# Performance work log

Measured on AMD Instinct MI355X. Metric: run time of the kernel, lower is better.

## Reference

```python
import jax, jax.numpy as jnp
import numpy as np

B, S, D, F, E, R, K = 1, 512, 1024, 4096, 8, 16, 2
SCALING = 32.0 / 16.0  # lora_alpha / lora_r
EPS = 1e-6


def setup_inputs() -> dict:
    key = jax.random.key(0)
    ks = jax.random.split(key, 12)
    w = lambda k, shape: jax.random.normal(k, shape, dtype=jnp.float32) * 0.02
    return {
        "x": jax.random.normal(ks[0], (B, S, D), dtype=jnp.float32),
        "norm_w": jnp.ones((D,), jnp.float32),
        "w1": w(ks[1], (F, D)),      # up proj (gate branch)
        "w3": w(ks[2], (F, D)),      # up proj (value branch)
        "w2": w(ks[3], (D, F)),      # down proj
        "gate_w": w(ks[4], (E, D)),  # router
        "a1": w(ks[5], (E, R, D)), "b1": w(ks[6], (E, F, R)),
        "a3": w(ks[7], (E, R, D)), "b3": w(ks[8], (E, F, R)),
        "a2": w(ks[9], (E, R, F)), "b2": w(ks[10], (E, D, R)),
    }


def _forward(x, norm_w, w1, w3, w2, gate_w, a1, b1, a3, b3, a2, b2):
    Bq, Sq, Dq = x.shape
    # RMSNorm
    nx = x * jax.lax.rsqrt(jnp.mean(x * x, axis=-1, keepdims=True) + EPS) * norm_w
    t = nx.reshape(-1, Dq)  # [T, D] flattened tokens
    # Mixtral-style routing: softmax -> top-k -> renormalize
    probs = jax.nn.softmax(t @ gate_w.T, axis=-1)          # [T, E]
    topw, topi = jax.lax.top_k(probs, K)                   # [T, K]
    topw = topw / jnp.sum(topw, axis=-1, keepdims=True)
    weights = jnp.sum(jax.nn.one_hot(topi, E, dtype=t.dtype) * topw[..., None], axis=1)  # [T, E]
    # Shared base up-projections
    base1 = t @ w1.T  # [T, F]
    base3 = t @ w3.T  # [T, F]
    # Per-expert LoRA deltas (rank-R): [E, T, F]
    h1 = base1[None] + SCALING * jnp.einsum('etr,efr->etf', jnp.einsum('td,erd->etr', t, a1), b1)
    h3 = base3[None] + SCALING * jnp.einsum('etr,efr->etf', jnp.einsum('td,erd->etr', t, a3), b3)
    act = jax.nn.silu(h1) * h3  # SwiGLU, [E, T, F]
    # Down projection: base + per-expert LoRA -> [E, T, D]
    out_e = jnp.einsum('etf,df->etd', act, w2) \
        + SCALING * jnp.einsum('etr,edr->etd', jnp.einsum('etf,erf->etr', act, a2), b2)
    # Weighted mix over experts (weight is 0 for non-selected experts)
    out = jnp.einsum('te,etd->td', weights, out_e)
    return out.reshape(Bq, Sq, Dq)


def reference(x, norm_w, w1, w3, w2, gate_w, a1, b1, a3, b3, a2, b2):
    return _forward(x, norm_w, w1, w3, w2, gate_w, a1, b1, a3, b3, a2, b2)
```

## Files before the change

### kernel.cpp

```cpp
#include <hip/hip_runtime.h>
#include <hip/hip_bf16.h>
#include <math.h>

#define TT 512
#define DD 1024
#define FF 4096
#define EE 8
#define RR 16
#define KKSEL 2
#define SCALING 2.0f
#define EPSV 1e-6f
#define DFC 128
#define SCHUNK 32
#define CVTB 1536

typedef unsigned short u16;
typedef short bhalf8 __attribute__((ext_vector_type(8)));
typedef float floatx4 __attribute__((ext_vector_type(4)));
typedef float f32x4 __attribute__((ext_vector_type(4)));
typedef unsigned short u16x8 __attribute__((ext_vector_type(8)));

__device__ __forceinline__ u16 f2b(float f) {
    unsigned x = __builtin_bit_cast(unsigned, f);
    unsigned r = (x + 0x7fffu + ((x >> 16) & 1u)) >> 16;
    return (u16)r;
}
__device__ __forceinline__ float b2f(u16 b) {
    unsigned x = ((unsigned)b) << 16;
    return __builtin_bit_cast(float, x);
}

__device__ __forceinline__ void gl_lds16(const void* g, void* l) {
    __builtin_amdgcn_global_load_lds(
        (const __attribute__((address_space(1))) void*)g,
        (__attribute__((address_space(3))) void*)l, 16, 0, 0);
}

__global__ __launch_bounds__(256) void prep_f2b_k(const float* __restrict__ x,
                                                  const float* __restrict__ nw,
                                                  const float* __restrict__ gw,
                                                  const float* __restrict__ a1,
                                                  const float* __restrict__ a3,
                                                  const float* __restrict__ w1,
                                                  const float* __restrict__ w3,
                                                  const float* __restrict__ w2,
                                                  u16* __restrict__ tb,
                                                  float* __restrict__ topw,
                                                  int* __restrict__ topi,
                                                  float* __restrict__ s1,
                                                  float* __restrict__ s3,
                                                  u16* __restrict__ wB) {
    __shared__ float tL[DD];
    __shared__ float red[12];
    __shared__ int sE[2];
    int tid = threadIdx.x;

    if (blockIdx.x < CVTB) {
        const int FD = FF * DD;
        int bid = blockIdx.x;
        int seg = bid >> 9;
        const float* src = (seg == 0) ? w1 : ((seg == 1) ? w3 : w2);
        u16* dst = wB + (size_t)seg * FD;
        int base = (bid & 511) * 8192;
        f32x4 v[8];
        #pragma unroll
        for (int j = 0; j < 8; j++)
            v[j] = __builtin_nontemporal_load((const f32x4*)(src + base + j * 1024) + tid);
        #pragma unroll
        for (int j = 0; j < 8; j++) {
            ushort4 o = { f2b(v[j][0]), f2b(v[j][1]), f2b(v[j][2]), f2b(v[j][3]) };
            *(ushort4*)(dst + base + j * 1024 + tid * 4) = o;
        }
        return;
    }

    int tok = blockIdx.x - CVTB;
    int wave = tid >> 6, lane = tid & 63;
    const float* xr = x + (size_t)tok * DD;
    float xv[4];
    float ss = 0.f;
    #pragma unroll
    for (int i = 0; i < 4; i++) { xv[i] = xr[tid + 256 * i]; ss += xv[i] * xv[i]; }
    #pragma unroll
    for (int o = 32; o > 0; o >>= 1) ss += __shfl_down(ss, o);
    if (lane == 0) red[wave] = ss;
    __syncthreads();
    if (tid == 0) red[8] = rsqrtf((red[0] + red[1] + red[2] + red[3]) * (1.0f / DD) + EPSV);
    __syncthreads();
    float rs = red[8];
    #pragma unroll
    for (int i = 0; i < 4; i++) {
        float v = xv[i] * rs * nw[tid + 256 * i];
        tL[tid + 256 * i] = v;
        tb[(size_t)tok * DD + tid + 256 * i] = f2b(v);
    }
    __syncthreads();
    {
        const float* g0 = gw + (size_t)(2 * wave) * DD;
        const float* g1 = g0 + DD;
        float a0 = 0.f, a1v = 0.f;
        for (int d = lane; d < DD; d += 64) {
            float tv = tL[d];
            a0 = fmaf(tv, g0[d], a0);
            a1v = fmaf(tv, g1[d], a1v);
        }
        #pragma unroll
        for (int o = 32; o > 0; o >>= 1) { a0 += __shfl_down(a0, o); a1v += __shfl_down(a1v, o); }
        if (lane == 0) { red[2 * wave] = a0; red[2 * wave + 1] = a1v; }
    }
    __syncthreads();
    if (tid == 0) {
        float m = red[0];
        #pragma unroll
        for (int e = 1; e < EE; e++) m = fmaxf(m, red[e]);
        float p[EE];
        #pragma unroll
        for (int e = 0; e < EE; e++) p[e] = expf(red[e] - m);
        int i0 = 0; float v0 = p[0];
        for (int e = 1; e < EE; e++) if (p[e] > v0) { v0 = p[e]; i0 = e; }
        int i1 = -1; float v1 = -1.f;
        for (int e = 0; e < EE; e++) { if (e == i0) continue; if (p[e] > v1) { v1 = p[e]; i1 = e; } }
        float inv = 1.f / (v0 + v1);
        topi[tok * KKSEL + 0] = i0;
        topi[tok * KKSEL + 1] = i1;
        topw[tok * KKSEL + 0] = v0 * inv;
        topw[tok * KKSEL + 1] = v1 * inv;
        sE[0] = i0; sE[1] = i1;
    }
    __syncthreads();
    {
        int half = wave >> 1, ten = wave & 1;
        int slot = tok * 2 + half;
        int e = sE[half];
        const float* ap = ten ? a3 : a1;
        float* sp = ten ? s3 : s1;
        float tv[16];
        #pragma unroll
        for (int i = 0; i < 16; i++) tv[i] = tL[lane + 64 * i];
        const float* ab = ap + (size_t)e * RR * DD;
        #pragma unroll
        for (int r = 0; r < RR; r++) {
            const float* ar = ab + (size_t)r * DD;
            float c = 0.f;
            #pragma unroll
            for (int i = 0; i < 16; i++) c = fmaf(tv[i], ar[lane + 64 * i], c);
            #pragma unroll
            for (int o = 32; o > 0; o >>= 1) c += __shfl_down(c, o);
            if (lane == 0) sp[slot * RR + r] = SCALING * c;
        }
    }
}

__global__ __launch_bounds__(256) void delta_act_k(const float* __restrict__ b1,
                                                   const float* __restrict__ b3,
                                                   const float* __restrict__ s1,
                                                   const float* __restrict__ s3,
                                                   const int* __restrict__ lists,
                                                   const int* __restrict__ counts,
                                                   const u16* __restrict__ hb,
                                                   u16* __restrict__ actb) {
    int e = blockIdx.y, f0 = blockIdx.x * DFC;
    int st = blockIdx.z * SCHUNK;
    int n = counts[e];
    if (st >= n) return;
    int gn = min(SCHUNK, n - st);
    __shared__ float bL[2][16 * 132];
    __shared__ float sG[2][SCHUNK * 16];
    __shared__ int   sSlot[SCHUNK];
    int tid = threadIdx.x;
    int g = tid >> 7, f = tid & 127;
    const int* lp = lists + e * 1024 + st;
    {
        const float* bsrc1 = b1 + ((size_t)e * FF + f0) * RR;
        const float* bsrc3 = b3 + ((size_t)e * FF + f0) * RR;
        #pragma unroll
        for (int i = tid; i < DFC * 16; i += 256) {
            int fi = i >> 4, r = i & 15;
            bL[0][r * 132 + fi] = bsrc1[i];
            bL[1][r * 132 + fi] = bsrc3[i];
        }
        int sl_l = (tid & 127) >> 2, q = tid & 3;
        if (sl_l < gn) {
            int slot = lp[sl_l];
            const float* ssrc = g ? s3 : s1;
            *(float4*)&sG[g][sl_l * 16 + q * 4] = *(const float4*)&ssrc[slot * RR + q * 4];
            if (g == 0 && q == 0) sSlot[sl_l] = slot;
        }
    }
    __syncthreads();
    for (int ii = g; ii < gn; ii += 2) {
        int slot = sSlot[ii];
        int tok = slot >> 1;
        float h1b = b2f(hb[(size_t)tok * (2 * FF) + f0 + f]);
        float h3b = b2f(hb[(size_t)tok * (2 * FF) + FF + f0 + f]);
        const float* sp1 = &sG[0][ii * 16];
        const float* sp3 = &sG[1][ii * 16];
        float d1 = 0.f, d3 = 0.f;
        #pragma unroll
        for (int r = 0; r < RR; r++) {
            d1 = fmaf(sp1[r], bL[0][r * 132 + f], d1);
            d3 = fmaf(sp3[r], bL[1][r * 132 + f], d3);
        }
        float h1 = h1b + d1, h3 = h3b + d3;
        float sig = 1.f / (1.f + expf(-h1));
        actb[(size_t)slot * FF + f0 + f] = f2b(h1 * sig * h3);
    }
}

template<int SPLITK, bool BF16OUT, bool LISTS>
__global__ __launch_bounds__(256) void gemm_nt(const u16* __restrict__ A,
                                               const u16* __restrict__ B,
                                               void* __restrict__ Cv,
                                               int M, int N, int K,
                                               const int* __restrict__ topi,
                                               int* __restrict__ lists,
                                               int* __restrict__ counts) {
    __shared__ u16 As[3][64 * 32];
    __shared__ u16 Bs[3][128 * 32];
    int tid = threadIdx.x;

    if (LISTS && blockIdx.y == gridDim.y - 1) {
        if (blockIdx.x == 0) {
            int* cnt = (int*)&As[0][0];
            if (tid < EE) cnt[tid] = 0;
            __syncthreads();
            for (int s = tid; s < TT * KKSEL; s += 256) atomicAdd(&cnt[topi[s]], 1);
            __syncthreads();
            if (tid < EE) { counts[tid] = cnt[tid]; cnt[tid] = 0; }
            __syncthreads();
            for (int s = tid; s < TT * KKSEL; s += 256) {
                int e = topi[s];
                int p = atomicAdd(&cnt[e], 1);
                lists[e * 1024 + p] = s;
            }
        }
        return;
    }

    int w = tid >> 6, lane = tid & 63;
    int wr = w >> 1, wc = w & 1;
    int lr = lane & 15, ks = lane >> 4;
    int z = (SPLITK > 1) ? blockIdx.z : 0;
    int kc = K / SPLITK;
    int k0s = z * kc;
    int nk = kc / 32;
    int m0 = blockIdx.y * 64, n0 = blockIdx.x * 128;

    int row = tid >> 2;
    int inb = (tid & 3) * 16;
    size_t rb = (size_t)K * 2;
    const char* Ag  = (const char*)A + (size_t)(m0 + row) * rb + inb + (size_t)k0s * 2;
    const char* Bg  = (const char*)B + (size_t)(n0 + row) * rb + inb + (size_t)k0s * 2;
    const char* Bg2 = Bg + 64 * rb;

    floatx4 zero4 = {0.f, 0.f, 0.f, 0.f};
    floatx4 acc[2][4];
    #pragma unroll
    for (int i = 0; i < 2; i++)
        #pragma unroll
        for (int j = 0; j < 4; j++) acc[i][j] = zero4;

    auto stage = [&](int buf, int kt) {
        size_t kb = (size_t)kt * 64;
        gl_lds16(Ag + kb, &As[buf][w * 512]);
        gl_lds16(Bg + kb, &Bs[buf][w * 512]);
        gl_lds16(Bg2 + kb, &Bs[buf][2048 + w * 512]);
    };
    auto compute = [&](int buf) {
        bhalf8 af[2], bf[4];
        #pragma unroll
        for (int i = 0; i < 2; i++)
            af[i] = *(const bhalf8*)&As[buf][(wr * 32 + i * 16 + lr) * 32 + ks * 8];
        #pragma unroll
        for (int j = 0; j < 4; j++)
            bf[j] = *(const bhalf8*)&Bs[buf][(wc * 64 + j * 16 + lr) * 32 + ks * 8];
        #pragma unroll
        for (int i = 0; i < 2; i++)
            #pragma unroll
            for (int j = 0; j < 4; j++)
                acc[i][j] = __builtin_amdgcn_mfma_f32_16x16x32_bf16(af[i], bf[j], acc[i][j], 0, 0, 0);
    };

    stage(0, 0);
    stage(1, 1);
    asm volatile("s_waitcnt vmcnt(3)" ::: "memory");
    __builtin_amdgcn_s_barrier();

    int cur = 0;
    for (int kt = 0; kt < nk; ++kt) {
        int pre = cur + 2; if (pre >= 3) pre -= 3;
        if (kt + 2 < nk) stage(pre, kt + 2);
        compute(cur);
        asm volatile("s_waitcnt lgkmcnt(0)" ::: "memory");
        if (kt + 1 < nk) {
            if (kt + 2 < nk) asm volatile("s_waitcnt vmcnt(3)" ::: "memory");
            else             asm volatile("s_waitcnt vmcnt(0)" ::: "memory");
            __builtin_amdgcn_s_barrier();
        }
        cur = (cur + 1 == 3) ? 0 : cur + 1;
    }

    int crow = (lane >> 4) * 4;
    #pragma unroll
    for (int i = 0; i < 2; i++) {
        #pragma unroll
        for (int j = 0; j < 4; j++) {
            int r0 = m0 + wr * 32 + i * 16 + crow;
            int c0 = n0 + wc * 64 + j * 16 + lr;
            if (BF16OUT) {
                u16* Cb = (u16*)Cv;
                #pragma unroll
                for (int mm = 0; mm < 4; mm++)
                    Cb[(size_t)(r0 + mm) * N + c0] = f2b(acc[i][j][mm]);
            } else {
                float* Cf = (float*)Cv + (size_t)z * M * N;
                #pragma unroll
                for (int mm = 0; mm < 4; mm++)
                    Cf[(size_t)(r0 + mm) * N + c0] = acc[i][j][mm];
            }
        }
    }
}

__global__ __launch_bounds__(256) void s2mix_k(const u16* __restrict__ actb,
                                               const float* __restrict__ a2,
                                               const int* __restrict__ topi,
                                               const float* __restrict__ topw,
                                               float* __restrict__ s2,
                                               u16* __restrict__ mixedb) {
    int tok = blockIdx.x;
    int tid = threadIdx.x, wave = tid >> 6, lane = tid & 63;
    int slot = tok * 2 + (wave >> 1);
    int e = topi[slot];
    const u16* ar = actb + (size_t)slot * FF;
    float av[64];
    #pragma unroll
    for (int i = 0; i < 16; i++) {
        ushort4 u = *(const ushort4*)(ar + lane * 4 + 256 * i);
        av[i * 4 + 0] = b2f(u.x); av[i * 4 + 1] = b2f(u.y);
        av[i * 4 + 2] = b2f(u.z); av[i * 4 + 3] = b2f(u.w);
    }
    #pragma unroll
    for (int rr = 0; rr < 8; rr++) {
        int r = (wave & 1) * 8 + rr;
        const float* a2p = a2 + ((size_t)e * RR + r) * FF;
        float c = 0.f;
        #pragma unroll
        for (int i = 0; i < 16; i++) {
            float4 w4 = *(const float4*)(a2p + lane * 4 + 256 * i);
            c = fmaf(av[i * 4 + 0], w4.x, c);
            c = fmaf(av[i * 4 + 1], w4.y, c);
            c = fmaf(av[i * 4 + 2], w4.z, c);
            c = fmaf(av[i * 4 + 3], w4.w, c);
        }
        #pragma unroll
        for (int o = 32; o > 0; o >>= 1) c += __shfl_down(c, o);
        if (lane == 0) s2[slot * RR + r] = SCALING * c;
    }
    float w0 = topw[tok * 2], w1v = topw[tok * 2 + 1];
    const u16* a0 = actb + (size_t)(tok * 2) * FF;
    const u16* a1p = a0 + FF;
    #pragma unroll
    for (int it = 0; it < 2; it++) {
        int f = tid * 8 + it * 2048;
        u16x8 v0 = *(const u16x8*)(a0 + f);
        u16x8 v1 = *(const u16x8*)(a1p + f);
        u16x8 o;
        #pragma unroll
        for (int q = 0; q < 8; q++)
            o[q] = f2b(w0 * b2f(v0[q]) + w1v * b2f(v1[q]));
        *(u16x8*)(mixedb + (size_t)tok * FF + f) = o;
    }
}

__global__ __launch_bounds__(256) void combine_k(const float* __restrict__ downP,
                                                 const float* __restrict__ s2,
                                                 const float* __restrict__ b2,
                                                 const float* __restrict__ topw,
                                                 const int* __restrict__ topi,
                                                 float* __restrict__ out) {
    int tok = blockIdx.x;
    for (int d = threadIdx.x; d < DD; d += 256) {
        float v = 0.f;
        #pragma unroll
        for (int zz = 0; zz < 8; zz++)
            v += downP[(size_t)zz * TT * DD + (size_t)tok * DD + d];
        #pragma unroll
        for (int k = 0; k < KKSEL; k++) {
            int slot = tok * KKSEL + k;
            int e = topi[slot];
            float w = topw[slot];
            const float* b2p = b2 + ((size_t)e * DD + d) * RR;
            const float* s2p = s2 + slot * RR;
            float l = 0.f;
            #pragma unroll
            for (int r = 0; r < RR; r++) l = fmaf(s2p[r], b2p[r], l);
            v += w * l;
        }
        out[(size_t)tok * DD + d] = v;
    }
}

extern "C" void kernel_launch(void* const* d_in, const int* in_sizes, int n_in,
                              void* d_out, int out_size, void* d_ws, size_t ws_size,
                              hipStream_t stream) {
    const float* x  = (const float*)d_in[0];
    const float* nw = (const float*)d_in[1];
    const float* w1 = (const float*)d_in[2];
    const float* w3 = (const float*)d_in[3];
    const float* w2 = (const float*)d_in[4];
    const float* gw = (const float*)d_in[5];
    const float* a1 = (const float*)d_in[6];
    const float* b1 = (const float*)d_in[7];
    const float* a3 = (const float*)d_in[8];
    const float* b3 = (const float*)d_in[9];
    const float* a2 = (const float*)d_in[10];
    const float* b2 = (const float*)d_in[11];
    float* out = (float*)d_out;

    float* downP = (float*)d_ws;
    float* s1    = downP + (size_t)8 * TT * DD;
    float* s3    = s1 + (size_t)TT * KKSEL * RR;
    float* s2    = s3 + (size_t)TT * KKSEL * RR;
    float* topw  = s2 + (size_t)TT * KKSEL * RR;
    int*   topi  = (int*)(topw + TT * KKSEL);
    int*   lists = topi + TT * KKSEL;
    int*   counts= lists + EE * 1024;
    u16*   tb    = (u16*)(counts + 16);
    u16*   wB    = tb + (size_t)TT * DD;
    u16*   w2b   = wB + (size_t)2 * FF * DD;
    u16*   hb    = w2b + (size_t)DD * FF;
    u16*   actb  = hb + (size_t)TT * 2 * FF;
    u16*   mixedb= actb + (size_t)TT * KKSEL * FF;

    prep_f2b_k<<<CVTB + TT, 256, 0, stream>>>(
        x, nw, gw, a1, a3, w1, w3, w2, tb, topw, topi, s1, s3, wB);
    gemm_nt<1, true, true><<<dim3(2 * FF / 128, TT / 64 + 1), 256, 0, stream>>>(
        tb, wB, hb, TT, 2 * FF, DD, topi, lists, counts);
    delta_act_k<<<dim3(FF / DFC, EE, 32), 256, 0, stream>>>(
        b1, b3, s1, s3, lists, counts, hb, actb);
    s2mix_k<<<TT, 256, 0, stream>>>(actb, a2, topi, topw, s2, mixedb);
    gemm_nt<8, false, false><<<dim3(DD / 128, TT / 64, 8), 256, 0, stream>>>(
        mixedb, w2b, downP, TT, DD, FF, nullptr, nullptr, nullptr);
    combine_k<<<TT, 256, 0, stream>>>(downP, s2, b2, topw, topi, out);
}
```

Baseline: 105.5 us.

## Fuse prep, weight conversion and up-projection GEMM into one persistent dataflow kernel

Merges the RMSNorm/routing prep kernel, the fp32-to-bf16 weight conversion and the first up-projection GEMM into a single kernel. Weight conversion becomes a work queue drained by all blocks. GEMM tiles spin on per-panel completion counters and a prep-done counter, so each tile can start as soon as its weight panel is converted instead of waiting at a kernel boundary. The expert list building moves into a dedicated block. This aims to overlap conversion with compute and cut launch gaps, but it adds inter-block spin-waits that assume co-residency (deadlock risk if the blocks are not scheduled together), plus atomic traffic and a memset.

```diff
diff --git a/kernel.cpp b/kernel.cpp
--- a/kernel.cpp
+++ b/kernel.cpp
@@ -12,7 +12,7 @@
 #define EPSV 1e-6f
 #define DFC 128
 #define SCHUNK 32
-#define CVTB 1536
+#define NQITEMS 1536
 
 typedef unsigned short u16;
 typedef short bhalf8 __attribute__((ext_vector_type(8)));
@@ -36,117 +36,262 @@
         (__attribute__((address_space(3))) void*)l, 16, 0, 0);
 }
 
-__global__ __launch_bounds__(256) void prep_f2b_k(const float* __restrict__ x,
-                                                  const float* __restrict__ nw,
-                                                  const float* __restrict__ gw,
-                                                  const float* __restrict__ a1,
-                                                  const float* __restrict__ a3,
-                                                  const float* __restrict__ w1,
-                                                  const float* __restrict__ w3,
-                                                  const float* __restrict__ w2,
-                                                  u16* __restrict__ tb,
-                                                  float* __restrict__ topw,
-                                                  int* __restrict__ topi,
-                                                  float* __restrict__ s1,
-                                                  float* __restrict__ s3,
-                                                  u16* __restrict__ wB) {
-    __shared__ float tL[DD];
+__global__ __launch_bounds__(256) void fused1_k(const float* __restrict__ x,
+                                                const float* __restrict__ nw,
+                                                const float* __restrict__ gw,
+                                                const float* __restrict__ a1,
+                                                const float* __restrict__ a3,
+                                                const float* __restrict__ w1,
+                                                const float* __restrict__ w3,
+                                                const float* __restrict__ w2,
+                                                u16* __restrict__ tb,
+                                                float* __restrict__ topw,
+                                                int* __restrict__ topi,
+                                                float* __restrict__ s1,
+                                                float* __restrict__ s3,
+                                                u16* __restrict__ wB,
+                                                u16* __restrict__ hb,
+                                                int* __restrict__ flags,
+                                                int* __restrict__ lists,
+                                                int* __restrict__ counts) {
+    __shared__ u16 sh[3 * 2048 + 3 * 4096];
+    __shared__ int qItS;
     __shared__ float red[12];
     __shared__ int sE[2];
     int tid = threadIdx.x;
-
-    if (blockIdx.x < CVTB) {
+    int bid = blockIdx.x;
+    int* qHead = flags;
+    int* prepDone = flags + 1;
+    int* panelCnt = flags + 64;
+
+    auto drain_queue = [&]() {
         const int FD = FF * DD;
-        int bid = blockIdx.x;
-        int seg = bid >> 9;
-        const float* src = (seg == 0) ? w1 : ((seg == 1) ? w3 : w2);
-        u16* dst = wB + (size_t)seg * FD;
-        int base = (bid & 511) * 8192;
-        f32x4 v[8];
-        #pragma unroll
-        for (int j = 0; j < 8; j++)
-            v[j] = __builtin_nontemporal_load((const f32x4*)(src + base + j * 1024) + tid);
-        #pragma unroll
-        for (int j = 0; j < 8; j++) {
-            ushort4 o = { f2b(v[j][0]), f2b(v[j][1]), f2b(v[j][2]), f2b(v[j][3]) };
-            *(ushort4*)(dst + base + j * 1024 + tid * 4) = o;
-        }
+        for (;;) {
+            if (tid == 0) qItS = atomicAdd(qHead, 1);
+            __syncthreads();
+            int it = qItS;
+            __syncthreads();
+            if (it >= NQITEMS) break;
+            const float* src;
+            u16* dst;
+            int p = -1;
+            if (it < 1024) {
+                p = it >> 4;
+                int row0 = p * 128 + (it & 15) * 8;
+                src = (row0 < FF) ? (w1 + (size_t)row0 * DD) : (w3 + (size_t)(row0 - FF) * DD);
+                dst = wB + (size_t)row0 * DD;
+            } else {
+                int c = it - 1024;
+                src = w2 + (size_t)c * 8192;
+                dst = wB + (size_t)2 * FD + (size_t)c * 8192;
+            }
+            f32x4 v[8];
+            #pragma unroll
+            for (int j = 0; j < 8; j++)
+                v[j] = __builtin_nontemporal_load((const f32x4*)(src + j * 1024) + tid);
+            #pragma unroll
+            for (int j = 0; j < 8; j++) {
+                ushort4 o = { f2b(v[j][0]), f2b(v[j][1]), f2b(v[j][2]), f2b(v[j][3]) };
+                *(ushort4*)(dst + j * 1024 + tid * 4) = o;
+            }
+            __syncthreads();
+            if (p >= 0 && tid == 0)
+                __hip_atomic_fetch_add(&panelCnt[p], 1, __ATOMIC_RELEASE, __HIP_MEMORY_SCOPE_AGENT);
+        }
+    };
+
+    if (bid < TT) {
+        int tok = bid;
+        int wave = tid >> 6, lane = tid & 63;
+        float* tL = (float*)sh;
+        const float* xr = x + (size_t)tok * DD;
+        float xv[4];
+        float ss = 0.f;
+        #pragma unroll
+        for (int i = 0; i < 4; i++) { xv[i] = xr[tid + 256 * i]; ss += xv[i] * xv[i]; }
+        #pragma unroll
+        for (int o = 32; o > 0; o >>= 1) ss += __shfl_down(ss, o);
+        if (lane == 0) red[wave] = ss;
+        __syncthreads();
+        if (tid == 0) red[8] = rsqrtf((red[0] + red[1] + red[2] + red[3]) * (1.0f / DD) + EPSV);
+        __syncthreads();
+        float rs = red[8];
+        #pragma unroll
+        for (int i = 0; i < 4; i++) {
+            float v = xv[i] * rs * nw[tid + 256 * i];
+            tL[tid + 256 * i] = v;
+            tb[(size_t)tok * DD + tid + 256 * i] = f2b(v);
+        }
+        __syncthreads();
+        {
+            const float* g0 = gw + (size_t)(2 * wave) * DD;
+            const float* g1 = g0 + DD;
+            float a0 = 0.f, a1v = 0.f;
+            for (int d = lane; d < DD; d += 64) {
+                float tv = tL[d];
+                a0 = fmaf(tv, g0[d], a0);
+                a1v = fmaf(tv, g1[d], a1v);
+            }
+            #pragma unroll
+            for (int o = 32; o > 0; o >>= 1) { a0 += __shfl_down(a0, o); a1v += __shfl_down(a1v, o); }
+            if (lane == 0) { red[2 * wave] = a0; red[2 * wave + 1] = a1v; }
+        }
+        __syncthreads();
+        if (tid == 0) {
+            float m = red[0];
+            #pragma unroll
+            for (int e = 1; e < EE; e++) m = fmaxf(m, red[e]);
+            float p[EE];
+            #pragma unroll
+            for (int e = 0; e < EE; e++) p[e] = expf(red[e] - m);
+            int i0 = 0; float v0 = p[0];
+            for (int e = 1; e < EE; e++) if (p[e] > v0) { v0 = p[e]; i0 = e; }
+            int i1 = -1; float v1 = -1.f;
+            for (int e = 0; e < EE; e++) { if (e == i0) continue; if (p[e] > v1) { v1 = p[e]; i1 = e; } }
+            float inv = 1.f / (v0 + v1);
+            topi[tok * KKSEL + 0] = i0;
+            topi[tok * KKSEL + 1] = i1;
+            topw[tok * KKSEL + 0] = v0 * inv;
+            topw[tok * KKSEL + 1] = v1 * inv;
+            sE[0] = i0; sE[1] = i1;
+        }
+        __syncthreads();
+        {
+            int half = wave >> 1, ten = wave & 1;
+            int slot = tok * 2 + half;
+            int e = sE[half];
+            const float* ap = ten ? a3 : a1;
+            float* sp = ten ? s3 : s1;
+            float tv[16];
+            #pragma unroll
+            for (int i = 0; i < 16; i++) tv[i] = tL[lane + 64 * i];
+            const float* ab = ap + (size_t)e * RR * DD;
+            #pragma unroll
+            for (int r = 0; r < RR; r++) {
+                const float* ar = ab + (size_t)r * DD;
+                float c = 0.f;
+                #pragma unroll
+                for (int i = 0; i < 16; i++) c = fmaf(tv[i], ar[lane + 64 * i], c);
+                #pragma unroll
+                for (int o = 32; o > 0; o >>= 1) c += __shfl_down(c, o);
+                if (lane == 0) sp[slot * RR + r] = SCALING * c;
+            }
+        }
+        __syncthreads();
+        if (tid == 0)
+            __hip_atomic_fetch_add(prepDone, 1, __ATOMIC_RELEASE, __HIP_MEMORY_SCOPE_AGENT);
+        drain_queue();
         return;
     }
 
-    int tok = blockIdx.x - CVTB;
-    int wave = tid >> 6, lane = tid & 63;
-    const float* xr = x + (size_t)tok * DD;
-    float xv[4];
-    float ss = 0.f;
-    #pragma unroll
-    for (int i = 0; i < 4; i++) { xv[i] = xr[tid + 256 * i]; ss += xv[i] * xv[i]; }
-    #pragma unroll
-    for (int o = 32; o > 0; o >>= 1) ss += __shfl_down(ss, o);
-    if (lane == 0) red[wave] = ss;
+    if (bid == TT + 512) {
+        drain_queue();
+        if (tid == 0) {
+            while (__hip_atomic_load(prepDone, __ATOMIC_ACQUIRE, __HIP_MEMORY_SCOPE_AGENT) < TT)
+                __builtin_amdgcn_s_sleep(8);
+        }
+        __syncthreads();
+        int* cnt = (int*)sh;
+        if (tid < EE) cnt[tid] = 0;
+        __syncthreads();
+        for (int s = tid; s < TT * KKSEL; s += 256) atomicAdd(&cnt[topi[s]], 1);
+        __syncthreads();
+        if (tid < EE) { counts[tid] = cnt[tid]; cnt[tid] = 0; }
+        __syncthreads();
+        for (int s = tid; s < TT * KKSEL; s += 256) {
+            int e = topi[s];
+            int p = atomicAdd(&cnt[e], 1);
+            lists[e * 1024 + p] = s;
+        }
+        return;
+    }
+
+    drain_queue();
+    int t = bid - TT;
+    int gx = t >> 3, gy = t & 7;
+    if (tid == 0) {
+        for (;;) {
+            int pc = __hip_atomic_load(&panelCnt[gx], __ATOMIC_ACQUIRE, __HIP_MEMORY_SCOPE_AGENT);
+            int pd = __hip_atomic_load(prepDone, __ATOMIC_ACQUIRE, __HIP_MEMORY_SCOPE_AGENT);
+            if (pc >= 16 && pd >= TT) break;
+            __builtin_amdgcn_s_sleep(8);
+        }
+    }
     __syncthreads();
-    if (tid == 0) red[8] = rsqrtf((red[0] + red[1] + red[2] + red[3]) * (1.0f / DD) + EPSV);
-    __syncthreads();
-    float rs = red[8];
-    #pragma unroll
-    for (int i = 0; i < 4; i++) {
-        float v = xv[i] * rs * nw[tid + 256 * i];
-        tL[tid + 256 * i] = v;
-        tb[(size_t)tok * DD + tid + 256 * i] = f2b(v);
-    }
-    __syncthreads();
-    {
-        const float* g0 = gw + (size_t)(2 * wave) * DD;
-        const float* g1 = g0 + DD;
-        float a0 = 0.f, a1v = 0.f;
-        for (int d = lane; d < DD; d += 64) {
-            float tv = tL[d];
-            a0 = fmaf(tv, g0[d], a0);
-            a1v = fmaf(tv, g1[d], a1v);
-        }
-        #pragma unroll
-        for (int o = 32; o > 0; o >>= 1) { a0 += __shfl_down(a0, o); a1v += __shfl_down(a1v, o); }
-        if (lane == 0) { red[2 * wave] = a0; red[2 * wave + 1] = a1v; }
-    }
-    __syncthreads();
-    if (tid == 0) {
-        float m = red[0];
-        #pragma unroll
-        for (int e = 1; e < EE; e++) m = fmaxf(m, red[e]);
-        float p[EE];
-        #pragma unroll
-        for (int e = 0; e < EE; e++) p[e] = expf(red[e] - m);
-        int i0 = 0; float v0 = p[0];
-        for (int e = 1; e < EE; e++) if (p[e] > v0) { v0 = p[e]; i0 = e; }
-        int i1 = -1; float v1 = -1.f;
-        for (int e = 0; e < EE; e++) { if (e == i0) continue; if (p[e] > v1) { v1 = p[e]; i1 = e; } }
-        float inv = 1.f / (v0 + v1);
-        topi[tok * KKSEL + 0] = i0;
-        topi[tok * KKSEL + 1] = i1;
-        topw[tok * KKSEL + 0] = v0 * inv;
-        topw[tok * KKSEL + 1] = v1 * inv;
-        sE[0] = i0; sE[1] = i1;
-    }
-    __syncthreads();
-    {
-        int half = wave >> 1, ten = wave & 1;
-        int slot = tok * 2 + half;
-        int e = sE[half];
-        const float* ap = ten ? a3 : a1;
-        float* sp = ten ? s3 : s1;
-        float tv[16];
-        #pragma unroll
-        for (int i = 0; i < 16; i++) tv[i] = tL[lane + 64 * i];
-        const float* ab = ap + (size_t)e * RR * DD;
-        #pragma unroll
-        for (int r = 0; r < RR; r++) {
-            const float* ar = ab + (size_t)r * DD;
-            float c = 0.f;
-            #pragma unroll
-            for (int i = 0; i < 16; i++) c = fmaf(tv[i], ar[lane + 64 * i], c);
-            #pragma unroll
-            for (int o = 32; o > 0; o >>= 1) c += __shfl_down(c, o);
-            if (lane == 0) sp[slot * RR + r] = SCALING * c;
+
+    u16* As = sh;
+    u16* Bs = sh + 3 * 2048;
+    int w = tid >> 6, lane = tid & 63;
+    int wr = w >> 1, wc = w & 1;
+    int lr = lane & 15, ks = lane >> 4;
+    const int K = DD, N = 2 * FF;
+    int nk = K / 32;
+    int m0 = gy * 64, n0 = gx * 128;
+
+    int row = tid >> 2;
+    int inb = (tid & 3) * 16;
+    size_t rb = (size_t)K * 2;
+    const char* Ag  = (const char*)tb + (size_t)(m0 + row) * rb + inb;
+    const char* Bg  = (const char*)wB + (size_t)(n0 + row) * rb + inb;
+    const char* Bg2 = Bg + 64 * rb;
+
+    floatx4 zero4 = {0.f, 0.f, 0.f, 0.f};
+    floatx4 acc[2][4];
+    #pragma unroll
+    for (int i = 0; i < 2; i++)
+        #pragma unroll
+        for (int j = 0; j < 4; j++) acc[i][j] = zero4;
+
+    auto stage = [&](int buf, int kt) {
+        size_t kb = (size_t)kt * 64;
+        gl_lds16(Ag + kb, &As[buf * 2048 + w * 512]);
+        gl_lds16(Bg + kb, &Bs[buf * 4096 + w * 512]);
+        gl_lds16(Bg2 + kb, &Bs[buf * 4096 + 2048 + w * 512]);
+    };
+    auto compute = [&](int buf) {
+        bhalf8 af[2], bf[4];
+        #pragma unroll
+        for (int i = 0; i < 2; i++)
+            af[i] = *(const bhalf8*)&As[buf * 2048 + (wr * 32 + i * 16 + lr) * 32 + ks * 8];
+        #pragma unroll
+        for (int j = 0; j < 4; j++)
+            bf[j] = *(const bhalf8*)&Bs[buf * 4096 + (wc * 64 + j * 16 + lr) * 32 + ks * 8];
+        #pragma unroll
+        for (int i = 0; i < 2; i++)
+            #pragma unroll
+            for (int j = 0; j < 4; j++)
+                acc[i][j] = __builtin_amdgcn_mfma_f32_16x16x32_bf16(af[i], bf[j], acc[i][j], 0, 0, 0);
+    };
+
+    stage(0, 0);
+    stage(1, 1);
+    asm volatile("s_waitcnt vmcnt(3)" ::: "memory");
+    __builtin_amdgcn_s_barrier();
+
+    int cur = 0;
+    for (int kt = 0; kt < nk; ++kt) {
+        int pre = cur + 2; if (pre >= 3) pre -= 3;
+        if (kt + 2 < nk) stage(pre, kt + 2);
+        compute(cur);
+        asm volatile("s_waitcnt lgkmcnt(0)" ::: "memory");
+        if (kt + 1 < nk) {
+            if (kt + 2 < nk) asm volatile("s_waitcnt vmcnt(3)" ::: "memory");
+            else             asm volatile("s_waitcnt vmcnt(0)" ::: "memory");
+            __builtin_amdgcn_s_barrier();
+        }
+        cur = (cur + 1 == 3) ? 0 : cur + 1;
+    }
+
+    int crow = (lane >> 4) * 4;
+    #pragma unroll
+    for (int i = 0; i < 2; i++) {
+        #pragma unroll
+        for (int j = 0; j < 4; j++) {
+            int r0 = m0 + wr * 32 + i * 16 + crow;
+            int c0 = n0 + wc * 64 + j * 16 + lr;
+            #pragma unroll
+            for (int mm = 0; mm < 4; mm++)
+                hb[(size_t)(r0 + mm) * N + c0] = f2b(acc[i][j][mm]);
         }
     }
 }
@@ -207,42 +352,18 @@
     }
 }
 
-template<int SPLITK, bool BF16OUT, bool LISTS>
-__global__ __launch_bounds__(256) void gemm_nt(const u16* __restrict__ A,
+__global__ __launch_bounds__(256) void gemm2_k(const u16* __restrict__ A,
                                                const u16* __restrict__ B,
-                                               void* __restrict__ Cv,
-                                               int M, int N, int K,
-                                               const int* __restrict__ topi,
-                                               int* __restrict__ lists,
-                                               int* __restrict__ counts) {
+                                               float* __restrict__ C0,
+                                               int M, int N, int K) {
     __shared__ u16 As[3][64 * 32];
     __shared__ u16 Bs[3][128 * 32];
     int tid = threadIdx.x;
-
-    if (LISTS && blockIdx.y == gridDim.y - 1) {
-        if (blockIdx.x == 0) {
-            int* cnt = (int*)&As[0][0];
-            if (tid < EE) cnt[tid] = 0;
-            __syncthreads();
-            for (int s = tid; s < TT * KKSEL; s += 256) atomicAdd(&cnt[topi[s]], 1);
-            __syncthreads();
-            if (tid < EE) { counts[tid] = cnt[tid]; cnt[tid] = 0; }
-            __syncthreads();
-            for (int s = tid; s < TT * KKSEL; s += 256) {
-                int e = topi[s];
-                int p = atomicAdd(&cnt[e], 1);
-                lists[e * 1024 + p] = s;
-            }
-        }
-        return;
-    }
-
     int w = tid >> 6, lane = tid & 63;
     int wr = w >> 1, wc = w & 1;
     int lr = lane & 15, ks = lane >> 4;
-    int z = (SPLITK > 1) ? blockIdx.z : 0;
-    int kc = K / SPLITK;
-    int k0s = z * kc;
+    int z = blockIdx.z;
+    int kc = K / 8, k0s = z * kc;
     int nk = kc / 32;
     int m0 = blockIdx.y * 64, n0 = blockIdx.x * 128;
 
@@ -300,6 +421,7 @@
         cur = (cur + 1 == 3) ? 0 : cur + 1;
     }
 
+    float* Cf = C0 + (size_t)z * M * N;
     int crow = (lane >> 4) * 4;
     #pragma unroll
     for (int i = 0; i < 2; i++) {
@@ -307,17 +429,9 @@
         for (int j = 0; j < 4; j++) {
             int r0 = m0 + wr * 32 + i * 16 + crow;
             int c0 = n0 + wc * 64 + j * 16 + lr;
-            if (BF16OUT) {
-                u16* Cb = (u16*)Cv;
-                #pragma unroll
-                for (int mm = 0; mm < 4; mm++)
-                    Cb[(size_t)(r0 + mm) * N + c0] = f2b(acc[i][j][mm]);
-            } else {
-                float* Cf = (float*)Cv + (size_t)z * M * N;
-                #pragma unroll
-                for (int mm = 0; mm < 4; mm++)
-                    Cf[(size_t)(r0 + mm) * N + c0] = acc[i][j][mm];
-            }
+            #pragma unroll
+            for (int mm = 0; mm < 4; mm++)
+                Cf[(size_t)(r0 + mm) * N + c0] = acc[i][j][mm];
         }
     }
 }
@@ -426,21 +540,22 @@
     int*   topi  = (int*)(topw + TT * KKSEL);
     int*   lists = topi + TT * KKSEL;
     int*   counts= lists + EE * 1024;
-    u16*   tb    = (u16*)(counts + 16);
+    int*   flags = counts + 16;
+    u16*   tb    = (u16*)(flags + 128);
     u16*   wB    = tb + (size_t)TT * DD;
     u16*   w2b   = wB + (size_t)2 * FF * DD;
     u16*   hb    = w2b + (size_t)DD * FF;
     u16*   actb  = hb + (size_t)TT * 2 * FF;
     u16*   mixedb= actb + (size_t)TT * KKSEL * FF;
 
-    prep_f2b_k<<<CVTB + TT, 256, 0, stream>>>(
-        x, nw, gw, a1, a3, w1, w3, w2, tb, topw, topi, s1, s3, wB);
-    gemm_nt<1, true, true><<<dim3(2 * FF / 128, TT / 64 + 1), 256, 0, stream>>>(
-        tb, wB, hb, TT, 2 * FF, DD, topi, lists, counts);
+    hipMemsetAsync(flags, 0, 128 * sizeof(int), stream);
+    fused1_k<<<TT + 512 + 1, 256, 0, stream>>>(
+        x, nw, gw, a1, a3, w1, w3, w2,
+        tb, topw, topi, s1, s3, wB, hb, flags, lists, counts);
     delta_act_k<<<dim3(FF / DFC, EE, 32), 256, 0, stream>>>(
         b1, b3, s1, s3, lists, counts, hb, actb);
     s2mix_k<<<TT, 256, 0, stream>>>(actb, a2, topi, topw, s2, mixedb);
-    gemm_nt<8, false, false><<<dim3(DD / 128, TT / 64, 8), 256, 0, stream>>>(
-        mixedb, w2b, downP, TT, DD, FF, nullptr, nullptr, nullptr);
+    gemm2_k<<<dim3(DD / 128, TT / 64, 8), 256, 0, stream>>>(
+        mixedb, w2b, downP, TT, DD, FF);
     combine_k<<<TT, 256, 0, stream>>>(downP, s2, b2, topw, topi, out);
 }
```

Result: slower. 256.2 us (+142.8%).
